# Kernel optimization log

Hardware: AMD Instinct MI355X
Metric: run time of the kernel (lower is better)

The kernel has to match this reference:

```python
import jax, jax.numpy as jnp
import numpy as np

B, T, D_MODEL, HEAD = 4, 4096, 1024, 64

def setup_inputs() -> dict:
    key = jax.random.key(0)
    kq, kk, kv, kwq, kwk, kwv = jax.random.split(key, 6)
    q = jax.random.normal(kq, (B, T, D_MODEL), dtype=jnp.float32)
    k = jax.random.normal(kk, (B, T, D_MODEL), dtype=jnp.float32)
    v = jax.random.normal(kv, (B, T, D_MODEL), dtype=jnp.float32)
    # causal mask: mask==0 positions are filled with -inf before softmax
    mask = jnp.tril(jnp.ones((T, T), dtype=jnp.int32))
    s = 1.0 / np.sqrt(D_MODEL)
    Wq = jax.random.normal(kwq, (D_MODEL, HEAD), dtype=jnp.float32) * s
    Wk = jax.random.normal(kwk, (D_MODEL, HEAD), dtype=jnp.float32) * s
    Wv = jax.random.normal(kwv, (D_MODEL, HEAD), dtype=jnp.float32) * s
    return {"q": q, "k": k, "v": v, "Wq": Wq, "Wk": Wk, "Wv": Wv, "mask": mask}

def reference(q, k, v, Wq, Wk, Wv, mask):
    # projections: [B,T,D] @ [D,H] -> [B,T,H]
    qh = jnp.einsum('btd,dh->bth', q, Wq)
    kh = jnp.einsum('btd,dh->bth', k, Wk)
    vh = jnp.einsum('btd,dh->bth', v, Wv)
    scale = jnp.float32(HEAD) ** 0.5
    # full score matrix [B,T,T] (faithful to naive implementation)
    scores = jnp.einsum('bqh,bkh->bqk', qh, kh) / scale
    scores = jnp.where(mask == 0, -jnp.inf, scores)
    weights = jax.nn.softmax(scores, axis=-1)
    out = jnp.einsum('bqk,bkh->bqh', weights, vh)  # [B,T,H]
    return out
```

## Files before the change

### kernel.cpp

```cpp
#include <hip/hip_runtime.h>
#include <hip/hip_bf16.h>

#define BB 4
#define TT 4096
#define DM 1024
#define HH 64
#define RTOT (BB * TT)
#define SLOTS_PER_B 144
#define CHUNK 512

typedef __attribute__((ext_vector_type(4))) float f32x4;
typedef __attribute__((ext_vector_type(16))) float f32x16;
typedef __attribute__((ext_vector_type(8))) short s16x8;

#define EXP2(x) __builtin_amdgcn_exp2f(x)

__device__ __forceinline__ ushort f2bf_bits(float f) {
    union { float f; unsigned u; } x;
    x.f = f;
    unsigned r = x.u + 0x7FFFu + ((x.u >> 16) & 1u);
    return (ushort)(r >> 16);
}

__device__ __forceinline__ unsigned pack2bf(float lo, float hi) {
    return (unsigned)f2bf_bits(lo) | ((unsigned)f2bf_bits(hi) << 16);
}

__device__ __forceinline__ void gld_lds16(const void* g, void* l) {
    __builtin_amdgcn_global_load_lds(
        (const __attribute__((address_space(1))) void*)g,
        (__attribute__((address_space(3))) void*)l, 16, 0, 0);
}

__global__ __launch_bounds__(256) void k_wtrans(const float* __restrict__ wq,
                                                const float* __restrict__ wk,
                                                const float* __restrict__ wv,
                                                ushort* __restrict__ wt) {
    int idx = blockIdx.x * 256 + threadIdx.x;
    int m = idx >> 16, e = idx & 65535;
    int kk = e >> 11, r = e & 2047;
    int f = r >> 9, s = r & 511;
    int l = s >> 3, j = s & 7;
    int col = (l & 15) + 16 * f;
    int kd  = kk * 32 + (l >> 4) * 8 + j;
    const float* W = (m == 0) ? wq : (m == 1) ? wk : wv;
    float v = W[kd * HH + col];
    if (m == 0) v *= 0.1803368801111204f;
    wt[idx] = f2bf_bits(v);
}

__global__ __launch_bounds__(512, 6) void k_proj(const float* __restrict__ q,
                                                 const float* __restrict__ k,
                                                 const float* __restrict__ v,
                                                 const ushort* __restrict__ wt,
                                                 ushort* __restrict__ qh,
                                                 ushort* __restrict__ kh,
                                                 ushort* __restrict__ vt) {
    int bid = blockIdx.x;
    int mat = bid >> 8;
    int rt  = bid & 255;
    const float* src = (mat == 0) ? q : (mat == 1) ? k : v;
    const ushort* w2 = wt + mat * 65536;

    __shared__ __align__(16) char ldsx[49152];

    int t = threadIdx.x;
    int w = t >> 6, l = t & 63, lr = l & 15, lg = l >> 4;
    int ws = w & 3, kh2 = w >> 2;
    int rbase = rt * 64;
    int ph = bid & 15;

    int ca = (l & 7) ^ ((l >> 3) & 7);
    const float* ag0 = src + (size_t)(rbase + ws * 16 + (l >> 3)) * DM + kh2 * 512 + ca * 4;
    const float* ag1 = ag0 + 8 * DM;
    char* abase = ldsx + w * 6144;

    int ax0 = (lr * 128 + lg * 32) ^ ((lr & 7) << 4);
    int wko = kh2 * 16;

    f32x4 acc[4] = {};
    s16x8 wA[4], wB[4];

#define KK(jj) ((((jj) + ph) & 15))
#define LOADW(dst, jj) do { int kk_ = wko + KK(jj);                               \
    dst[0] = *reinterpret_cast<const s16x8*>(w2 + (kk_ * 4 + 0) * 512 + l * 8);   \
    dst[1] = *reinterpret_cast<const s16x8*>(w2 + (kk_ * 4 + 1) * 512 + l * 8);   \
    dst[2] = *reinterpret_cast<const s16x8*>(w2 + (kk_ * 4 + 2) * 512 + l * 8);   \
    dst[3] = *reinterpret_cast<const s16x8*>(w2 + (kk_ * 4 + 3) * 512 + l * 8); } while (0)
#define STAGEA(jj) do { int ko_ = KK(jj) * 32; int bo_ = ((jj) % 3) * 2048;       \
    gld_lds16(ag0 + ko_, abase + bo_);                                            \
    gld_lds16(ag1 + ko_, abase + bo_ + 1024); } while (0)

    LOADW(wA, 0); STAGEA(0);
    LOADW(wB, 1); STAGEA(1);

#define BODY(jj, WCUR, VM) do {                                                   \
    asm volatile("s_waitcnt vmcnt(" #VM ")" ::: "memory");                        \
    __builtin_amdgcn_sched_barrier(0);                                            \
    {                                                                             \
        const char* ab = abase + ((jj) % 3) * 2048;                               \
        f32x4 av0 = *reinterpret_cast<const f32x4*>(ab + ax0);                    \
        f32x4 av1 = *reinterpret_cast<const f32x4*>(ab + (ax0 ^ 16));             \
        s16x8 af;                                                                 \
        af[0] = f2bf_bits(av0[0]); af[1] = f2bf_bits(av0[1]);                     \
        af[2] = f2bf_bits(av0[2]); af[3] = f2bf_bits(av0[3]);                     \
        af[4] = f2bf_bits(av1[0]); af[5] = f2bf_bits(av1[1]);                     \
        af[6] = f2bf_bits(av1[2]); af[7] = f2bf_bits(av1[3]);                     \
        acc[0] = __builtin_amdgcn_mfma_f32_16x16x32_bf16(af, WCUR[0], acc[0], 0, 0, 0); \
        acc[1] = __builtin_amdgcn_mfma_f32_16x16x32_bf16(af, WCUR[1], acc[1], 0, 0, 0); \
        acc[2] = __builtin_amdgcn_mfma_f32_16x16x32_bf16(af, WCUR[2], acc[2], 0, 0, 0); \
        acc[3] = __builtin_amdgcn_mfma_f32_16x16x32_bf16(af, WCUR[3], acc[3], 0, 0, 0); \
    }                                                                             \
    __builtin_amdgcn_sched_barrier(0);                                            \
    if ((jj) + 2 < 16) { LOADW(WCUR, (jj) + 2); STAGEA((jj) + 2); }               \
} while (0)

    BODY(0,  wA, 6);  BODY(1,  wB, 6);  BODY(2,  wA, 6);  BODY(3,  wB, 6);
    BODY(4,  wA, 6);  BODY(5,  wB, 6);  BODY(6,  wA, 6);  BODY(7,  wB, 6);
    BODY(8,  wA, 6);  BODY(9,  wB, 6);  BODY(10, wA, 6);  BODY(11, wB, 6);
    BODY(12, wA, 6);  BODY(13, wB, 6);  BODY(14, wA, 6);  BODY(15, wB, 0);
#undef BODY
#undef STAGEA
#undef LOADW
#undef KK

    __syncthreads();
    float* xb = (float*)ldsx;
    if (kh2 == 1) {
#pragma unroll
        for (int f = 0; f < 4; ++f)
#pragma unroll
            for (int r = 0; r < 4; ++r)
                xb[ws * 1040 + (lg * 4 + r) * 65 + lr + 16 * f] = acc[f][r];
    }
    __syncthreads();
    if (kh2 == 0) {
#pragma unroll
        for (int f = 0; f < 4; ++f)
#pragma unroll
            for (int r = 0; r < 4; ++r) {
                float sum = acc[f][r] + xb[ws * 1040 + (lg * 4 + r) * 65 + lr + 16 * f];
                int row = rbase + ws * 16 + lg * 4 + r;
                int col = lr + 16 * f;
                ushort bv = f2bf_bits(sum);
                if (mat == 0)      qh[row * HH + col] = bv;
                else if (mat == 1) kh[row * HH + col] = bv;
                else               vt[(size_t)col * RTOT + row] = bv;
            }
    }
}

__global__ __launch_bounds__(256, 2) void k_attn(const ushort* __restrict__ qh,
                                                 const ushort* __restrict__ kh,
                                                 const ushort* __restrict__ vt,
                                                 float* __restrict__ pm,
                                                 float* __restrict__ pl,
                                                 float* __restrict__ pO) {
    int c = blockIdx.x, qt = blockIdx.y, b = blockIdx.z;
    int a = qt >> 2, r = qt & 3;
    int nch = a + 1;
    if (c >= nch) return;
    int slot = b * SLOTS_PER_B + 2 * a * (a + 1) + r * (a + 1) + c;

    __shared__ __align__(16) ushort kbuf[2][2048];
    __shared__ __align__(16) ushort vbuf[2][2048];

    int t = threadIdx.x, w = t >> 6, l = t & 63, lq = l & 31, hf = l >> 5;
    int W0 = qt * 128 + w * 32;
    size_t bT = (size_t)b * TT;
    int kv0 = c * CHUNK;
    int kvend = min(kv0 + CHUNK, (qt + 1) * 128);
    int nsteps = (kvend - kv0) >> 5;
    bool diag = (c == nch - 1);

    s16x8 qf[4];
#pragma unroll
    for (int s = 0; s < 4; ++s)
        qf[s] = *reinterpret_cast<const s16x8*>(qh + (bT + W0 + lq) * HH + s * 16 + hf * 8);

    int krow = t >> 3, kch = t & 7;
    int vrow = t >> 2, vch = t & 3;
    const ushort* kgp = kh + (bT + kv0 + krow) * HH + kch * 8;
    const ushort* vgp = vt + (size_t)vrow * RTOT + bT + kv0 + vch * 8;
    int kwo = (krow * 128 + kch * 16) ^ ((krow & 7) << 4);
    int vwo = (vrow * 64 + vch * 16) ^ ((vrow & 7) << 4);

    uint4 ks = *reinterpret_cast<const uint4*>(kgp);
    uint4 vs = *reinterpret_cast<const uint4*>(vgp);
    *reinterpret_cast<uint4*>(reinterpret_cast<char*>(&kbuf[0][0]) + kwo) = ks;
    *reinterpret_cast<uint4*>(reinterpret_cast<char*>(&vbuf[0][0]) + vwo) = vs;

    float m = -1e30f, ssum = 0.f;
    f32x16 oacc0 = {}, oacc1 = {};

    for (int j = 0; j < nsteps; ++j) {
        int cur = j & 1;
        if (j + 1 < nsteps) {
            ks = *reinterpret_cast<const uint4*>(kgp + (j + 1) * 32 * HH);
            vs = *reinterpret_cast<const uint4*>(vgp + (j + 1) * 32);
        }
        __syncthreads();
        int kvb = kv0 + j * 32;
        bool skip = diag && (kvb > W0 + 31);
        if (!skip) {
            const char* kb_ = reinterpret_cast<const char*>(&kbuf[cur][0]);
            const char* vb_ = reinterpret_cast<const char*>(&vbuf[cur][0]);
            f32x16 sacc = {};
#pragma unroll
            for (int s = 0; s < 4; ++s) {
                int ko = (lq * 128 + s * 32 + hf * 16) ^ ((lq & 7) << 4);
                s16x8 kf = *reinterpret_cast<const s16x8*>(kb_ + ko);
                sacc = __builtin_amdgcn_mfma_f32_32x32x16_bf16(kf, qf[s], sacc, 0, 0, 0);
            }
            if (diag && (kvb + 31 > W0)) {
                int qcol = W0 + lq;
#pragma unroll
                for (int g = 0; g < 16; ++g) {
                    int kvr = kvb + (g & 3) + 8 * (g >> 2) + 4 * hf;
                    if (kvr > qcol) sacc[g] = -1e30f;
                }
            }
            float t0 = fmaxf(fmaxf(fmaxf(sacc[0], sacc[1]), fmaxf(sacc[2], sacc[3])),
                             fmaxf(fmaxf(sacc[4], sacc[5]), fmaxf(sacc[6], sacc[7])));
            float t1 = fmaxf(fmaxf(fmaxf(sacc[8], sacc[9]), fmaxf(sacc[10], sacc[11])),
                             fmaxf(fmaxf(sacc[12], sacc[13]), fmaxf(sacc[14], sacc[15])));
            float tmx = fmaxf(t0, t1);
            tmx = fmaxf(tmx, __shfl_xor(tmx, 32));
            float mnew = fmaxf(m, tmx);
            float corr = EXP2(m - mnew);
            float p[16];
#pragma unroll
            for (int g = 0; g < 16; ++g) p[g] = EXP2(sacc[g] - mnew);
            float ts = ((p[0] + p[1]) + (p[2] + p[3])) + ((p[4] + p[5]) + (p[6] + p[7]))
                     + ((p[8] + p[9]) + (p[10] + p[11])) + ((p[12] + p[13]) + (p[14] + p[15]));
            ts += __shfl_xor(ts, 32);
            ssum = ssum * corr + ts;
            m = mnew;
#pragma unroll
            for (int g = 0; g < 16; ++g) { oacc0[g] *= corr; oacc1[g] *= corr; }
            unsigned d0 = pack2bf(p[0], p[1]),   d1 = pack2bf(p[2], p[3]);
            unsigned d2 = pack2bf(p[4], p[5]),   d3 = pack2bf(p[6], p[7]);
            unsigned d4 = pack2bf(p[8], p[9]),   d5 = pack2bf(p[10], p[11]);
            unsigned d6 = pack2bf(p[12], p[13]), d7 = pack2bf(p[14], p[15]);
            unsigned s0 = __shfl_xor(d0, 32), s1 = __shfl_xor(d1, 32);
            unsigned s2 = __shfl_xor(d2, 32), s3 = __shfl_xor(d3, 32);
            unsigned s4 = __shfl_xor(d4, 32), s5 = __shfl_xor(d5, 32);
            unsigned s6 = __shfl_xor(d6, 32), s7 = __shfl_xor(d7, 32);
            union { unsigned u[4]; s16x8 v; } pf0, pf1;
            pf0.u[0] = hf ? s2 : d0;  pf0.u[1] = hf ? s3 : d1;
            pf0.u[2] = hf ? d2 : s0;  pf0.u[3] = hf ? d3 : s1;
            pf1.u[0] = hf ? s6 : d4;  pf1.u[1] = hf ? s7 : d5;
            pf1.u[2] = hf ? d6 : s4;  pf1.u[3] = hf ? d7 : s5;
#pragma unroll
            for (int ts2 = 0; ts2 < 2; ++ts2) {
                int vo0 = ((0 * 32 + lq) * 64 + ts2 * 32 + hf * 16) ^ ((lq & 7) << 4);
                int vo1 = ((1 * 32 + lq) * 64 + ts2 * 32 + hf * 16) ^ ((lq & 7) << 4);
                s16x8 vf0 = *reinterpret_cast<const s16x8*>(vb_ + vo0);
                s16x8 vf1 = *reinterpret_cast<const s16x8*>(vb_ + vo1);
                s16x8 pf = ts2 ? pf1.v : pf0.v;
                oacc0 = __builtin_amdgcn_mfma_f32_32x32x16_bf16(vf0, pf, oacc0, 0, 0, 0);
                oacc1 = __builtin_amdgcn_mfma_f32_32x32x16_bf16(vf1, pf, oacc1, 0, 0, 0);
            }
        }
        __syncthreads();
        if (j + 1 < nsteps) {
            *reinterpret_cast<uint4*>(reinterpret_cast<char*>(&kbuf[cur ^ 1][0]) + kwo) = ks;
            *reinterpret_cast<uint4*>(reinterpret_cast<char*>(&vbuf[cur ^ 1][0]) + vwo) = vs;
        }
    }

    if (l < 32) {
        pm[(size_t)slot * 128 + w * 32 + l] = m;
        pl[(size_t)slot * 128 + w * 32 + l] = ssum;
    }
    float* po = pO + (size_t)slot * 8192;
#pragma unroll
    for (int g = 0; g < 16; ++g) {
        int hrow = (g & 3) + 8 * (g >> 2) + 4 * hf;
        po[hrow * 128 + w * 32 + lq] = oacc0[g];
        po[(32 + hrow) * 128 + w * 32 + lq] = oacc1[g];
    }
}

__global__ __launch_bounds__(256) void k_merge(const float* __restrict__ pm,
                                               const float* __restrict__ pl,
                                               const float* __restrict__ pO,
                                               float* __restrict__ out) {
    int qt = blockIdx.x & 31, b = blockIdx.x >> 5;
    int a = qt >> 2, r = qt & 3, nch = a + 1;
    int slot0 = b * SLOTS_PER_B + 2 * a * (a + 1) + r * (a + 1);

    __shared__ float wgt[8][128];
    __shared__ float invl[128];
    __shared__ float tr[64][130];

    int t = threadIdx.x;
    if (t < 128) {
        float M = -3e38f;
        for (int cc = 0; cc < nch; ++cc)
            M = fmaxf(M, pm[(size_t)(slot0 + cc) * 128 + t]);
        float L = 0.f;
        for (int cc = 0; cc < nch; ++cc) {
            float g = EXP2(pm[(size_t)(slot0 + cc) * 128 + t] - M);
            wgt[cc][t] = g;
            L += pl[(size_t)(slot0 + cc) * 128 + t] * g;
        }
        invl[t] = 1.0f / L;
    }
    __syncthreads();

    float4 acc[8] = {};
    for (int cc = 0; cc < nch; ++cc) {
        const float4* pp = reinterpret_cast<const float4*>(pO + (size_t)(slot0 + cc) * 8192);
#pragma unroll
        for (int it = 0; it < 8; ++it) {
            int idx = it * 256 + t, h = idx >> 5, qc = idx & 31;
            float4 vv = pp[h * 32 + qc];
            float4 w4 = *reinterpret_cast<const float4*>(&wgt[cc][qc * 4]);
            acc[it].x += vv.x * w4.x; acc[it].y += vv.y * w4.y;
            acc[it].z += vv.z * w4.z; acc[it].w += vv.w * w4.w;
        }
    }
#pragma unroll
    for (int it = 0; it < 8; ++it) {
        int idx = it * 256 + t, h = idx >> 5, qc = idx & 31;
        tr[h][qc * 4 + 0] = acc[it].x * invl[qc * 4 + 0];
        tr[h][qc * 4 + 1] = acc[it].y * invl[qc * 4 + 1];
        tr[h][qc * 4 + 2] = acc[it].z * invl[qc * 4 + 2];
        tr[h][qc * 4 + 3] = acc[it].w * invl[qc * 4 + 3];
    }
    __syncthreads();

    int q = t >> 1, half = t & 1;
    size_t obase = ((size_t)b * TT + qt * 128 + q) * 64 + half * 32;
#pragma unroll
    for (int jj = 0; jj < 8; ++jj) {
        float4 o;
        o.x = tr[half * 32 + jj * 4 + 0][q];
        o.y = tr[half * 32 + jj * 4 + 1][q];
        o.z = tr[half * 32 + jj * 4 + 2][q];
        o.w = tr[half * 32 + jj * 4 + 3][q];
        *reinterpret_cast<float4*>(out + obase + jj * 4) = o;
    }
}

extern "C" void kernel_launch(void* const* d_in, const int* in_sizes, int n_in,
                              void* d_out, int out_size, void* d_ws, size_t ws_size,
                              hipStream_t stream) {
    const float* q  = (const float*)d_in[0];
    const float* k  = (const float*)d_in[1];
    const float* v  = (const float*)d_in[2];
    const float* wq = (const float*)d_in[3];
    const float* wk = (const float*)d_in[4];
    const float* wv = (const float*)d_in[5];
    float* out = (float*)d_out;

    char* ws = (char*)d_ws;
    ushort* qh = (ushort*)(ws);
    ushort* kh = (ushort*)(ws + (2ull << 20));
    ushort* vt = (ushort*)(ws + (4ull << 20));
    ushort* wt = (ushort*)(ws + (6ull << 20));
    float*  pm = (float*)(ws + (7ull << 20));
    float*  pl = (float*)(ws + (7ull << 20) + (512u << 10));
    float*  pO = (float*)(ws + (8ull << 20));

    k_wtrans<<<768, 256, 0, stream>>>(wq, wk, wv, wt);
    k_proj<<<768, 512, 0, stream>>>(q, k, v, wt, qh, kh, vt);
    k_attn<<<dim3(8, 32, 4), 256, 0, stream>>>(qh, kh, vt, pm, pl, pO);
    k_merge<<<128, 256, 0, stream>>>(pm, pl, pO, out);
}
```

Baseline: 87.84 us.

## Halve KV chunk size for more split-K blocks and store partial outputs in bf16

The KV chunk size per attention block drops from 512 to 256. This doubles the number of split-K work items, so the causal grid fills the GPU more evenly, and the slot indexing, grid dimensions and merge weight buffer are updated to match. Partial outputs are now written as bf16 instead of fp32, and the merge kernel converts them back, which halves partial-output traffic now that there are twice as many partials. The trade-offs are more merge work, extra partial m/l writes, and reduced precision in the partial accumulators.

```diff
diff --git a/kernel.cpp b/kernel.cpp
--- a/kernel.cpp
+++ b/kernel.cpp
@@ -6,8 +6,8 @@
 #define DM 1024
 #define HH 64
 #define RTOT (BB * TT)
-#define SLOTS_PER_B 144
-#define CHUNK 512
+#define SLOTS_PER_B 272
+#define CHUNK 256
 
 typedef __attribute__((ext_vector_type(4))) float f32x4;
 typedef __attribute__((ext_vector_type(16))) float f32x16;
@@ -20,6 +20,12 @@
     x.f = f;
     unsigned r = x.u + 0x7FFFu + ((x.u >> 16) & 1u);
     return (ushort)(r >> 16);
+}
+
+__device__ __forceinline__ float bf2f(ushort u) {
+    union { unsigned i; float f; } x;
+    x.i = ((unsigned)u) << 16;
+    return x.f;
 }
 
 __device__ __forceinline__ unsigned pack2bf(float lo, float hi) {
@@ -155,12 +161,12 @@
                                                  const ushort* __restrict__ vt,
                                                  float* __restrict__ pm,
                                                  float* __restrict__ pl,
-                                                 float* __restrict__ pO) {
+                                                 ushort* __restrict__ pO) {
     int c = blockIdx.x, qt = blockIdx.y, b = blockIdx.z;
-    int a = qt >> 2, r = qt & 3;
-    int nch = a + 1;
+    int m_ = qt >> 1, e_ = qt & 1;
+    int nch = m_ + 1;
     if (c >= nch) return;
-    int slot = b * SLOTS_PER_B + 2 * a * (a + 1) + r * (a + 1) + c;
+    int slot = b * SLOTS_PER_B + m_ * (m_ + 1) + e_ * (m_ + 1) + c;
 
     __shared__ __align__(16) ushort kbuf[2][2048];
     __shared__ __align__(16) ushort vbuf[2][2048];
@@ -273,24 +279,24 @@
         pm[(size_t)slot * 128 + w * 32 + l] = m;
         pl[(size_t)slot * 128 + w * 32 + l] = ssum;
     }
-    float* po = pO + (size_t)slot * 8192;
+    ushort* po = pO + (size_t)slot * 8192;
 #pragma unroll
     for (int g = 0; g < 16; ++g) {
         int hrow = (g & 3) + 8 * (g >> 2) + 4 * hf;
-        po[hrow * 128 + w * 32 + lq] = oacc0[g];
-        po[(32 + hrow) * 128 + w * 32 + lq] = oacc1[g];
+        po[hrow * 128 + w * 32 + lq] = f2bf_bits(oacc0[g]);
+        po[(32 + hrow) * 128 + w * 32 + lq] = f2bf_bits(oacc1[g]);
     }
 }
 
 __global__ __launch_bounds__(256) void k_merge(const float* __restrict__ pm,
                                                const float* __restrict__ pl,
-                                               const float* __restrict__ pO,
+                                               const ushort* __restrict__ pO,
                                                float* __restrict__ out) {
     int qt = blockIdx.x & 31, b = blockIdx.x >> 5;
-    int a = qt >> 2, r = qt & 3, nch = a + 1;
-    int slot0 = b * SLOTS_PER_B + 2 * a * (a + 1) + r * (a + 1);
-
-    __shared__ float wgt[8][128];
+    int m_ = qt >> 1, e_ = qt & 1, nch = m_ + 1;
+    int slot0 = b * SLOTS_PER_B + m_ * (m_ + 1) + e_ * (m_ + 1);
+
+    __shared__ float wgt[16][128];
     __shared__ float invl[128];
     __shared__ float tr[64][130];
 
@@ -309,25 +315,28 @@
     }
     __syncthreads();
 
-    float4 acc[8] = {};
+    float acc[32] = {};
     for (int cc = 0; cc < nch; ++cc) {
-        const float4* pp = reinterpret_cast<const float4*>(pO + (size_t)(slot0 + cc) * 8192);
+        const ushort* pp = pO + (size_t)(slot0 + cc) * 8192;
 #pragma unroll
         for (int it = 0; it < 8; ++it) {
-            int idx = it * 256 + t, h = idx >> 5, qc = idx & 31;
-            float4 vv = pp[h * 32 + qc];
-            float4 w4 = *reinterpret_cast<const float4*>(&wgt[cc][qc * 4]);
-            acc[it].x += vv.x * w4.x; acc[it].y += vv.y * w4.y;
-            acc[it].z += vv.z * w4.z; acc[it].w += vv.w * w4.w;
+            int e = it * 1024 + t * 4;
+            int qc = e & 127;
+            ushort4 v4 = *reinterpret_cast<const ushort4*>(pp + e);
+            acc[it * 4 + 0] += bf2f(v4.x) * wgt[cc][qc + 0];
+            acc[it * 4 + 1] += bf2f(v4.y) * wgt[cc][qc + 1];
+            acc[it * 4 + 2] += bf2f(v4.z) * wgt[cc][qc + 2];
+            acc[it * 4 + 3] += bf2f(v4.w) * wgt[cc][qc + 3];
         }
     }
 #pragma unroll
     for (int it = 0; it < 8; ++it) {
-        int idx = it * 256 + t, h = idx >> 5, qc = idx & 31;
-        tr[h][qc * 4 + 0] = acc[it].x * invl[qc * 4 + 0];
-        tr[h][qc * 4 + 1] = acc[it].y * invl[qc * 4 + 1];
-        tr[h][qc * 4 + 2] = acc[it].z * invl[qc * 4 + 2];
-        tr[h][qc * 4 + 3] = acc[it].w * invl[qc * 4 + 3];
+        int e = it * 1024 + t * 4;
+        int h = e >> 7, qc = e & 127;
+        tr[h][qc + 0] = acc[it * 4 + 0] * invl[qc + 0];
+        tr[h][qc + 1] = acc[it * 4 + 1] * invl[qc + 1];
+        tr[h][qc + 2] = acc[it * 4 + 2] * invl[qc + 2];
+        tr[h][qc + 3] = acc[it * 4 + 3] * invl[qc + 3];
     }
     __syncthreads();
 
@@ -361,11 +370,11 @@
     ushort* vt = (ushort*)(ws + (4ull << 20));
     ushort* wt = (ushort*)(ws + (6ull << 20));
     float*  pm = (float*)(ws + (7ull << 20));
-    float*  pl = (float*)(ws + (7ull << 20) + (512u << 10));
-    float*  pO = (float*)(ws + (8ull << 20));
+    float*  pl = (float*)(ws + (8ull << 20));
+    ushort* pO = (ushort*)(ws + (9ull << 20));
 
     k_wtrans<<<768, 256, 0, stream>>>(wq, wk, wv, wt);
     k_proj<<<768, 512, 0, stream>>>(q, k, v, wt, qh, kh, vt);
-    k_attn<<<dim3(8, 32, 4), 256, 0, stream>>>(qh, kh, vt, pm, pl, pO);
+    k_attn<<<dim3(16, 32, 4), 256, 0, stream>>>(qh, kh, vt, pm, pl, pO);
     k_merge<<<128, 256, 0, stream>>>(pm, pl, pO, out);
 }
```

Result: slower. 91.32 us (+4.0%).
